# Performance work log

Hardware: AMD Instinct MI355X
Metric: run time of the kernel (lower is better)

## Reference

```python
import jax, jax.numpy as jnp
import numpy as np

E = 8        # numExperts
D = 1024     # d_model
F = 4096     # expert hidden = 4*d_model
T = 8192     # total tokens (sum of expertFrequency)


def setup_inputs() -> dict:
    key = jax.random.key(0)
    k0, k1, k2, k3, k4 = jax.random.split(key, 5)
    expertOrderedInput = jax.random.normal(k0, (T, D), dtype=jnp.float32)
    # Static equal split so the split sizes are jit-compatible.
    expertFrequency = jnp.full((E,), T // E, dtype=jnp.int64)
    s1 = 1.0 / np.sqrt(D)
    s2 = 1.0 / np.sqrt(F)
    w1 = jax.random.normal(k1, (E, D, F), dtype=jnp.float32) * s1
    b1 = jnp.zeros((E, F), dtype=jnp.float32)
    w2 = jax.random.normal(k2, (E, F, D), dtype=jnp.float32) * s2
    b2 = jnp.zeros((E, D), dtype=jnp.float32)
    return {"expertOrderedInput": expertOrderedInput,
            "expertFrequency": expertFrequency,
            "w1": w1, "b1": b1, "w2": w2, "b2": b2}


def reference(expertOrderedInput, expertFrequency, w1, b1, w2, b2):
    # expertOrderedInput: [T, D], tokens pre-sorted by expert.
    # expertFrequency is equal per expert (T/E each), so the
    # split-loop-cat in the torch module is exactly a grouped GEMM.
    e = w1.shape[0]
    t = expertOrderedInput.shape[0]
    x = expertOrderedInput.reshape(e, t // e, -1)            # [E, T/E, D]
    h = jax.nn.gelu(jnp.einsum('etd,edf->etf', x, w1) + b1[:, None, :])
    y = jnp.einsum('etf,efd->etd', h, w2) + b2[:, None, :]   # [E, T/E, D]
    return y.reshape(t, -1)                                   # cat along dim 0
```

## Files before the change

kernel.cpp:

```cpp
#include <hip/hip_runtime.h>

#define E_ 8
#define D_ 1024
#define F_ 4096
#define T_ 8192

typedef unsigned short u16;
typedef short bf16x8 __attribute__((ext_vector_type(8)));
typedef float f32x4 __attribute__((ext_vector_type(4)));
typedef unsigned short u16x8 __attribute__((ext_vector_type(8)));
typedef unsigned short u16x2 __attribute__((ext_vector_type(2)));

__device__ __forceinline__ u16 f2bf(float f) {
    unsigned u = __builtin_bit_cast(unsigned, f);
    u += 0x7fffu + ((u >> 16) & 1u);
    return (u16)(u >> 16);
}

__device__ __forceinline__ float gelu_fast(float x) {
    const float a = -2.885390082f * 0.7978845608028654f;
    const float b = a * 0.044715f;
    float u = x * x;
    float p = x * __builtin_fmaf(b, u, a);
    float e = exp2f(p);
    return x * __builtin_amdgcn_rcpf(1.0f + e);
}

__device__ __forceinline__ void async16(const void* g, void* l) {
    __builtin_amdgcn_global_load_lds(
        (const __attribute__((address_space(1))) unsigned int*)g,
        (__attribute__((address_space(3))) unsigned int*)l, 16, 0, 0);
}

__global__ void cvt_x(const float* __restrict__ in, u16* __restrict__ out) {
    int i = blockIdx.x * 256 + threadIdx.x;
    const float4* in4 = (const float4*)in;
    float4 a = in4[2 * i], b = in4[2 * i + 1];
    u16x8 o;
    o[0] = f2bf(a.x); o[1] = f2bf(a.y); o[2] = f2bf(a.z); o[3] = f2bf(a.w);
    o[4] = f2bf(b.x); o[5] = f2bf(b.y); o[6] = f2bf(b.z); o[7] = f2bf(b.w);
    *(u16x8*)(out + (size_t)i * 8) = o;
}

__global__ __launch_bounds__(256) void transpose_cvt(
    const float* __restrict__ src, u16* __restrict__ dst, int R, int C) {
    __shared__ float tile[32][129];
    int e = blockIdx.z;
    src += (size_t)e * R * C;
    dst += (size_t)e * R * C;
    int c0 = blockIdx.x * 32, r0 = blockIdx.y * 128;
    int tid = threadIdx.x;
    int lc = tid & 31, lr0 = tid >> 5;
#pragma unroll
    for (int i = 0; i < 16; ++i) {
        int r = lr0 + i * 8;
        tile[lc][r] = src[(size_t)(r0 + r) * C + c0 + lc];
    }
    __syncthreads();
    int sc = tid >> 6, sr = (tid & 63) * 2;
#pragma unroll
    for (int i = 0; i < 8; ++i) {
        int c = sc + i * 4;
        u16x2 v;
        v[0] = f2bf(tile[c][sr]);
        v[1] = f2bf(tile[c][sr + 1]);
        *(u16x2*)(dst + (size_t)(c0 + c) * R + r0 + sr) = v;
    }
}

template <int BN, int EPI, int NM, int NN>
__global__ __launch_bounds__(512, 2) void gemm2p(
    const u16* __restrict__ A,
    const u16* __restrict__ Bt,
    const float* __restrict__ bias,
    void* __restrict__ Cv,
    int Mpe, int N, int K) {
    constexpr int BM  = 256;
    constexpr int LA  = 2;
    constexpr int LB  = BN / 128;
    constexpr int MFR = 4;
    constexpr int NFR = BN / 32;
    constexpr int NH  = NFR / 2;
    constexpr int AELEM = 4 * BM * 32;
    constexpr int VMS = LA + LB;
    constexpr int RDS = MFR + 2 * NH;
    constexpr int LGP = MFR + NH;
    __shared__ u16 lds[AELEM + 4 * BN * 32];

    const int tid = threadIdx.x;
    const int w = tid >> 6, lane = tid & 63;
    const int lr = lane & 15, lg = lane >> 4;
    const int wm = w >> 1, wn = w & 1;

    constexpr int NWG = E_ * NM * NN;
    constexpr int PER = NWG / 8;
    const int bid = blockIdx.x;
    const int logical = (bid & 7) * PER + (bid >> 3);
    const int e   = logical / (NM * NN);
    const int rem = logical % (NM * NN);
    const int bn  = rem / NM;
    const int bm  = rem % NM;

    A    += (size_t)e * Mpe * K;
    Bt   += (size_t)e * N * K;
    bias += (size_t)e * N;
    const int n0 = bn * BN;
    const int m0 = bm * BM;
    const int NT = K >> 6;

    const char* gA[LA];
    const char* gB[LB];
    {
        int kch = (lane & 3) ^ ((lane >> 3) & 3);
#pragma unroll
        for (int i = 0; i < LA; ++i) {
            int row = i * 128 + w * 16 + (lane >> 2);
            gA[i] = (const char*)(A + (size_t)(m0 + row) * K + kch * 8);
        }
#pragma unroll
        for (int i = 0; i < LB; ++i) {
            int row = i * 128 + w * 16 + (lane >> 2);
            gB[i] = (const char*)(Bt + (size_t)(n0 + row) * K + kch * 8);
        }
    }
    char* ldsc = (char*)lds;

    auto stageA = [&](int t, int h) {
        size_t goff = (size_t)t * 128 + (size_t)h * 64;
        unsigned dst = (unsigned)((((t & 1) * 2 + h) * (BM * 64)) + w * 1024);
#pragma unroll
        for (int i = 0; i < LA; ++i)
            async16(gA[i] + goff, ldsc + dst + i * 8192);
    };
    auto stageB = [&](int t, int h) {
        size_t goff = (size_t)t * 128 + (size_t)h * 64;
        unsigned dst = (unsigned)(AELEM * 2 + (((t & 1) * 2 + h) * (BN * 64)) + w * 1024);
#pragma unroll
        for (int i = 0; i < LB; ++i)
            async16(gB[i] + goff, ldsc + dst + i * 8192);
    };

    f32x4 acc[MFR][NFR];
    const f32x4 zero = {0.f, 0.f, 0.f, 0.f};
#pragma unroll
    for (int i = 0; i < MFR; ++i)
#pragma unroll
        for (int j = 0; j < NFR; ++j) acc[i][j] = zero;

    const u16* SBb = lds + AELEM;
    const int arow = wm * 64 + lr;
    const int nbase = wn * (BN / 2) + lr;
    const int axor = (lg ^ ((arow >> 1) & 3)) * 8;
    const int bxor = (lg ^ ((nbase >> 1) & 3)) * 8;

    bf16x8 aC[MFR], aN[MFR], bloA[NH], bloB[NH], bhi[NH];

    stageA(0, 0); stageB(0, 0); stageA(0, 1); stageB(0, 1);
    if (NT > 1) { stageA(1, 0); stageB(1, 0); }
    if (NT > 1) asm volatile("s_waitcnt vmcnt(%0)" :: "i"(VMS) : "memory");
    else        asm volatile("s_waitcnt vmcnt(0)" ::: "memory");
    __builtin_amdgcn_s_barrier();
    __builtin_amdgcn_sched_barrier(0);
#pragma unroll
    for (int i = 0; i < MFR; ++i)
        aC[i] = *(const bf16x8*)(lds + (arow + i * 16) * 32 + axor);
#pragma unroll
    for (int j = 0; j < NH; ++j)
        bloA[j] = *(const bf16x8*)(SBb + (nbase + j * 16) * 32 + bxor);
    __builtin_amdgcn_sched_barrier(0);

#define MFMA_SUB(AARR, BARR, J0)                                              \
    __builtin_amdgcn_s_setprio(1);                                            \
    _Pragma("unroll")                                                         \
    for (int i = 0; i < MFR; ++i) {                                           \
        _Pragma("unroll")                                                     \
        for (int j = 0; j < NH; ++j)                                          \
            acc[i][(J0) + j] = __builtin_amdgcn_mfma_f32_16x16x32_bf16(       \
                AARR[i], BARR[j], acc[i][(J0) + j], 0, 0, 0);                 \
    }                                                                         \
    __builtin_amdgcn_s_setprio(0);

#pragma unroll 2
    for (int c = 0; c < NT; ++c) {
        const int bb = c & 1;
        const u16* SA1 = lds + (bb * 2 + 1) * (BM * 32);
        const u16* SB0 = SBb + (bb * 2 + 0) * (BN * 32);
        const u16* SB1 = SBb + (bb * 2 + 1) * (BN * 32);
        const u16* SA0n = lds + ((bb ^ 1) * 2) * (BM * 32);
        const u16* SB0n = SBb + ((bb ^ 1) * 2) * (BN * 32);
        const bool stg1 = (c + 1 < NT);
        const bool stg2 = (c + 2 < NT);

#pragma unroll
        for (int j = 0; j < NH; ++j)
            bhi[j] = *(const bf16x8*)(SB0 + (nbase + (NH + j) * 16) * 32 + bxor);
#pragma unroll
        for (int i = 0; i < MFR; ++i)
            aN[i] = *(const bf16x8*)(SA1 + (arow + i * 16) * 32 + axor);
#pragma unroll
        for (int j = 0; j < NH; ++j)
            bloB[j] = *(const bf16x8*)(SB1 + (nbase + j * 16) * 32 + bxor);
        if (stg1) { stageA(c + 1, 1); stageB(c + 1, 1); }
        __builtin_amdgcn_sched_barrier(0);
        asm volatile("s_waitcnt lgkmcnt(%0)" :: "i"(RDS) : "memory");
        __builtin_amdgcn_sched_barrier(0);
        MFMA_SUB(aC, bloA, 0);
        __builtin_amdgcn_sched_barrier(0);
        asm volatile("s_waitcnt lgkmcnt(%0)" :: "i"(LGP) : "memory");
        __builtin_amdgcn_sched_barrier(0);
        MFMA_SUB(aC, bhi, NH);
        __builtin_amdgcn_sched_barrier(0);
        if (stg1) asm volatile("s_waitcnt vmcnt(%0)" :: "i"(VMS) : "memory");
        else      asm volatile("s_waitcnt vmcnt(0)" ::: "memory");
        __builtin_amdgcn_s_barrier();
        __builtin_amdgcn_sched_barrier(0);

#pragma unroll
        for (int j = 0; j < NH; ++j)
            bhi[j] = *(const bf16x8*)(SB1 + (nbase + (NH + j) * 16) * 32 + bxor);
        if (stg1) {
#pragma unroll
            for (int i = 0; i < MFR; ++i)
                aC[i] = *(const bf16x8*)(SA0n + (arow + i * 16) * 32 + axor);
#pragma unroll
            for (int j = 0; j < NH; ++j)
                bloA[j] = *(const bf16x8*)(SB0n + (nbase + j * 16) * 32 + bxor);
        }
        if (stg2) { stageA(c + 2, 0); stageB(c + 2, 0); }
        __builtin_amdgcn_sched_barrier(0);
        if (stg1) asm volatile("s_waitcnt lgkmcnt(%0)" :: "i"(RDS) : "memory");
        else      asm volatile("s_waitcnt lgkmcnt(%0)" :: "i"(NH) : "memory");
        __builtin_amdgcn_sched_barrier(0);
        MFMA_SUB(aN, bloB, 0);
        __builtin_amdgcn_sched_barrier(0);
        if (stg1) asm volatile("s_waitcnt lgkmcnt(%0)" :: "i"(LGP) : "memory");
        else      asm volatile("s_waitcnt lgkmcnt(0)" ::: "memory");
        __builtin_amdgcn_sched_barrier(0);
        MFMA_SUB(aN, bhi, NH);
        __builtin_amdgcn_sched_barrier(0);
        if (stg2) asm volatile("s_waitcnt vmcnt(%0)" :: "i"(VMS) : "memory");
        else      asm volatile("s_waitcnt vmcnt(0)" ::: "memory");
        __builtin_amdgcn_s_barrier();
        __builtin_amdgcn_sched_barrier(0);
    }
#undef MFMA_SUB

    const int mb = m0 + wm * 64, nb = n0 + wn * (BN / 2);
    if constexpr (EPI == 1) {
        u16* C = (u16*)Cv + (size_t)e * Mpe * N;
#pragma unroll
        for (int i = 0; i < MFR; ++i) {
#pragma unroll
            for (int j = 0; j < NFR; ++j) {
                int col = nb + j * 16 + lr;
                float bv = bias[col];
                int row = mb + i * 16 + lg * 4;
#pragma unroll
                for (int t = 0; t < 4; ++t) {
                    float v = acc[i][j][t] + bv;
                    C[(size_t)(row + t) * N + col] = f2bf(gelu_fast(v));
                }
            }
        }
    } else {
        float* C = (float*)Cv + (size_t)e * Mpe * N;
#pragma unroll
        for (int i = 0; i < MFR; ++i) {
#pragma unroll
            for (int j = 0; j < NFR; ++j) {
                int col = nb + j * 16 + lr;
                float bv = bias[col];
                int row = mb + i * 16 + lg * 4;
#pragma unroll
                for (int t = 0; t < 4; ++t)
                    C[(size_t)(row + t) * N + col] = acc[i][j][t] + bv;
            }
        }
    }
}

extern "C" void kernel_launch(void* const* d_in, const int* in_sizes, int n_in,
                              void* d_out, int out_size, void* d_ws, size_t ws_size,
                              hipStream_t stream) {
    const float* X  = (const float*)d_in[0];
    const float* w1 = (const float*)d_in[2];
    const float* b1 = (const float*)d_in[3];
    const float* w2 = (const float*)d_in[4];
    const float* b2 = (const float*)d_in[5];
    float* out = (float*)d_out;

    const size_t XBF_B = (size_t)T_ * D_ * 2;
    const size_t WT_B  = (size_t)E_ * F_ * D_ * 2;
    const size_t H_B   = (size_t)T_ * F_ * 2;
    if (ws_size < XBF_B + WT_B + H_B) return;

    char* ws = (char*)d_ws;
    u16* Xbf = (u16*)ws;
    u16* Wt  = (u16*)(ws + XBF_B);
    u16* H   = (u16*)(ws + XBF_B + WT_B);

    cvt_x<<<dim3((T_ * D_) / 8 / 256), dim3(256), 0, stream>>>(X, Xbf);
    transpose_cvt<<<dim3(F_ / 32, D_ / 128, E_), dim3(256), 0, stream>>>(w1, Wt, D_, F_);
    gemm2p<256, 1, 4, 16><<<dim3(512), dim3(512), 0, stream>>>(
        Xbf, Wt, b1, H, T_ / E_, F_, D_);
    transpose_cvt<<<dim3(D_ / 32, F_ / 128, E_), dim3(256), 0, stream>>>(w2, Wt, F_, D_);
    gemm2p<128, 0, 4, 8><<<dim3(256), dim3(512), 0, stream>>>(
        H, Wt, b2, out, T_ / E_, D_, F_);
}
```

Baseline: 243.3 us.

## Fuse weight transpose and bf16 conversion into GEMM B-tile staging

Removes the two transpose_cvt kernels. The GEMMs now read fp32 weights directly from global memory into registers, convert them with v_cvt_pk_bf16_f32, and write them swizzled into LDS inside the software pipeline. This saves the extra passes over 256 MB of fp32 weights plus the write and re-read of the bf16 transposed copy. In exchange, each GEMM block re-reads fp32 weights (twice the bytes, once per M tile), loses the async global-to-LDS path for B, and adds register pressure and VALU work.

```diff
diff --git a/kernel.cpp b/kernel.cpp
--- a/kernel.cpp
+++ b/kernel.cpp
@@ -9,12 +9,18 @@
 typedef short bf16x8 __attribute__((ext_vector_type(8)));
 typedef float f32x4 __attribute__((ext_vector_type(4)));
 typedef unsigned short u16x8 __attribute__((ext_vector_type(8)));
-typedef unsigned short u16x2 __attribute__((ext_vector_type(2)));
+typedef unsigned int u32x4 __attribute__((ext_vector_type(4)));
 
 __device__ __forceinline__ u16 f2bf(float f) {
     unsigned u = __builtin_bit_cast(unsigned, f);
     u += 0x7fffu + ((u >> 16) & 1u);
     return (u16)(u >> 16);
+}
+
+__device__ __forceinline__ unsigned cvtpk(float a, float b) {
+    unsigned d;
+    asm("v_cvt_pk_bf16_f32 %0, %1, %2" : "=v"(d) : "v"(a), "v"(b));
+    return d;
 }
 
 __device__ __forceinline__ float gelu_fast(float x) {
@@ -42,49 +48,23 @@
     *(u16x8*)(out + (size_t)i * 8) = o;
 }
 
-__global__ __launch_bounds__(256) void transpose_cvt(
-    const float* __restrict__ src, u16* __restrict__ dst, int R, int C) {
-    __shared__ float tile[32][129];
-    int e = blockIdx.z;
-    src += (size_t)e * R * C;
-    dst += (size_t)e * R * C;
-    int c0 = blockIdx.x * 32, r0 = blockIdx.y * 128;
-    int tid = threadIdx.x;
-    int lc = tid & 31, lr0 = tid >> 5;
-#pragma unroll
-    for (int i = 0; i < 16; ++i) {
-        int r = lr0 + i * 8;
-        tile[lc][r] = src[(size_t)(r0 + r) * C + c0 + lc];
-    }
-    __syncthreads();
-    int sc = tid >> 6, sr = (tid & 63) * 2;
-#pragma unroll
-    for (int i = 0; i < 8; ++i) {
-        int c = sc + i * 4;
-        u16x2 v;
-        v[0] = f2bf(tile[c][sr]);
-        v[1] = f2bf(tile[c][sr + 1]);
-        *(u16x2*)(dst + (size_t)(c0 + c) * R + r0 + sr) = v;
-    }
-}
-
 template <int BN, int EPI, int NM, int NN>
-__global__ __launch_bounds__(512, 2) void gemm2p(
+__global__ __launch_bounds__(512, 2) void gemm2pw(
     const u16* __restrict__ A,
-    const u16* __restrict__ Bt,
+    const float* __restrict__ W,
     const float* __restrict__ bias,
     void* __restrict__ Cv,
     int Mpe, int N, int K) {
     constexpr int BM  = 256;
     constexpr int LA  = 2;
-    constexpr int LB  = BN / 128;
     constexpr int MFR = 4;
     constexpr int NFR = BN / 32;
     constexpr int NH  = NFR / 2;
+    constexpr int UNITS = BN / 128;
     constexpr int AELEM = 4 * BM * 32;
-    constexpr int VMS = LA + LB;
-    constexpr int RDS = MFR + 2 * NH;
-    constexpr int LGP = MFR + NH;
+    constexpr int RD  = MFR + 2 * NH;
+    constexpr int ENTRY = RD + UNITS;
+    constexpr int MID = MFR + NH;
     __shared__ u16 lds[AELEM + 4 * BN * 32];
 
     const int tid = threadIdx.x;
@@ -102,14 +82,13 @@
     const int bm  = rem % NM;
 
     A    += (size_t)e * Mpe * K;
-    Bt   += (size_t)e * N * K;
+    W    += (size_t)e * K * N;
     bias += (size_t)e * N;
     const int n0 = bn * BN;
     const int m0 = bm * BM;
     const int NT = K >> 6;
 
     const char* gA[LA];
-    const char* gB[LB];
     {
         int kch = (lane & 3) ^ ((lane >> 3) & 3);
 #pragma unroll
@@ -117,11 +96,6 @@
             int row = i * 128 + w * 16 + (lane >> 2);
             gA[i] = (const char*)(A + (size_t)(m0 + row) * K + kch * 8);
         }
-#pragma unroll
-        for (int i = 0; i < LB; ++i) {
-            int row = i * 128 + w * 16 + (lane >> 2);
-            gB[i] = (const char*)(Bt + (size_t)(n0 + row) * K + kch * 8);
-        }
     }
     char* ldsc = (char*)lds;
 
@@ -132,12 +106,34 @@
         for (int i = 0; i < LA; ++i)
             async16(gA[i] + goff, ldsc + dst + i * 8192);
     };
-    auto stageB = [&](int t, int h) {
-        size_t goff = (size_t)t * 128 + (size_t)h * 64;
-        unsigned dst = (unsigned)(AELEM * 2 + (((t & 1) * 2 + h) * (BN * 64)) + w * 1024);
-#pragma unroll
-        for (int i = 0; i < LB; ++i)
-            async16(gB[i] + goff, ldsc + dst + i * 8192);
+
+    const int NBLK = w & (BN / 64 - 1);
+    const int OCT0 = (w / (BN / 64)) * UNITS;
+    const int nl = NBLK * 64 + lane;
+    const float* Wb = W + n0 + nl;
+    float fb[UNITS * 8];
+
+    auto loadB = [&](int t, int h) {
+#pragma unroll
+        for (int u = 0; u < UNITS; ++u)
+#pragma unroll
+            for (int j = 0; j < 8; ++j) {
+                int row = t * 64 + h * 32 + (OCT0 + u) * 8 + j;
+                fb[u * 8 + j] = Wb[(size_t)row * N];
+            }
+    };
+    const int bwswz = ((nl >> 1) & 3);
+    auto writeB = [&](int t, int h) {
+        unsigned base = (unsigned)(AELEM * 2 + (((t & 1) * 2 + h) * (BN * 64)));
+#pragma unroll
+        for (int u = 0; u < UNITS; ++u) {
+            u32x4 v;
+            v[0] = cvtpk(fb[u * 8 + 0], fb[u * 8 + 1]);
+            v[1] = cvtpk(fb[u * 8 + 2], fb[u * 8 + 3]);
+            v[2] = cvtpk(fb[u * 8 + 4], fb[u * 8 + 5]);
+            v[3] = cvtpk(fb[u * 8 + 6], fb[u * 8 + 7]);
+            *(u32x4*)(ldsc + base + nl * 64 + (((OCT0 + u) ^ bwswz) << 4)) = v;
+        }
     };
 
     f32x4 acc[MFR][NFR];
@@ -155,10 +151,15 @@
 
     bf16x8 aC[MFR], aN[MFR], bloA[NH], bloB[NH], bhi[NH];
 
-    stageA(0, 0); stageB(0, 0); stageA(0, 1); stageB(0, 1);
-    if (NT > 1) { stageA(1, 0); stageB(1, 0); }
-    if (NT > 1) asm volatile("s_waitcnt vmcnt(%0)" :: "i"(VMS) : "memory");
-    else        asm volatile("s_waitcnt vmcnt(0)" ::: "memory");
+    loadB(0, 0);
+    asm volatile("s_waitcnt vmcnt(0)" ::: "memory");
+    writeB(0, 0);
+    loadB(0, 1);
+    asm volatile("s_waitcnt vmcnt(0)" ::: "memory");
+    writeB(0, 1);
+    loadB(1, 0);
+    stageA(0, 0); stageA(0, 1); stageA(1, 0);
+    asm volatile("s_waitcnt vmcnt(0)" ::: "memory");
     __builtin_amdgcn_s_barrier();
     __builtin_amdgcn_sched_barrier(0);
 #pragma unroll
@@ -180,7 +181,6 @@
     }                                                                         \
     __builtin_amdgcn_s_setprio(0);
 
-#pragma unroll 2
     for (int c = 0; c < NT; ++c) {
         const int bb = c & 1;
         const u16* SA1 = lds + (bb * 2 + 1) * (BM * 32);
@@ -191,6 +191,7 @@
         const bool stg1 = (c + 1 < NT);
         const bool stg2 = (c + 2 < NT);
 
+        if (stg1) { writeB(c + 1, 0); loadB(c + 1, 1); }
 #pragma unroll
         for (int j = 0; j < NH; ++j)
             bhi[j] = *(const bf16x8*)(SB0 + (nbase + (NH + j) * 16) * 32 + bxor);
@@ -200,21 +201,24 @@
 #pragma unroll
         for (int j = 0; j < NH; ++j)
             bloB[j] = *(const bf16x8*)(SB1 + (nbase + j * 16) * 32 + bxor);
-        if (stg1) { stageA(c + 1, 1); stageB(c + 1, 1); }
-        __builtin_amdgcn_sched_barrier(0);
-        asm volatile("s_waitcnt lgkmcnt(%0)" :: "i"(RDS) : "memory");
+        if (stg1) stageA(c + 1, 1);
+        __builtin_amdgcn_sched_barrier(0);
+        if (stg1) asm volatile("s_waitcnt lgkmcnt(%0)" :: "i"(ENTRY) : "memory");
+        else      asm volatile("s_waitcnt lgkmcnt(%0)" :: "i"(RD) : "memory");
         __builtin_amdgcn_sched_barrier(0);
         MFMA_SUB(aC, bloA, 0);
         __builtin_amdgcn_sched_barrier(0);
-        asm volatile("s_waitcnt lgkmcnt(%0)" :: "i"(LGP) : "memory");
+        asm volatile("s_waitcnt lgkmcnt(%0)" :: "i"(MID) : "memory");
         __builtin_amdgcn_sched_barrier(0);
         MFMA_SUB(aC, bhi, NH);
         __builtin_amdgcn_sched_barrier(0);
-        if (stg1) asm volatile("s_waitcnt vmcnt(%0)" :: "i"(VMS) : "memory");
+        if (stg1) asm volatile("s_waitcnt vmcnt(2)" ::: "memory");
         else      asm volatile("s_waitcnt vmcnt(0)" ::: "memory");
         __builtin_amdgcn_s_barrier();
         __builtin_amdgcn_sched_barrier(0);
 
+        if (stg1) writeB(c + 1, 1);
+        if (stg2) loadB(c + 2, 0);
 #pragma unroll
         for (int j = 0; j < NH; ++j)
             bhi[j] = *(const bf16x8*)(SB1 + (nbase + (NH + j) * 16) * 32 + bxor);
@@ -226,19 +230,19 @@
             for (int j = 0; j < NH; ++j)
                 bloA[j] = *(const bf16x8*)(SB0n + (nbase + j * 16) * 32 + bxor);
         }
-        if (stg2) { stageA(c + 2, 0); stageB(c + 2, 0); }
-        __builtin_amdgcn_sched_barrier(0);
-        if (stg1) asm volatile("s_waitcnt lgkmcnt(%0)" :: "i"(RDS) : "memory");
+        if (stg2) stageA(c + 2, 0);
+        __builtin_amdgcn_sched_barrier(0);
+        if (stg1) asm volatile("s_waitcnt lgkmcnt(%0)" :: "i"(ENTRY) : "memory");
         else      asm volatile("s_waitcnt lgkmcnt(%0)" :: "i"(NH) : "memory");
         __builtin_amdgcn_sched_barrier(0);
         MFMA_SUB(aN, bloB, 0);
         __builtin_amdgcn_sched_barrier(0);
-        if (stg1) asm volatile("s_waitcnt lgkmcnt(%0)" :: "i"(LGP) : "memory");
+        if (stg1) asm volatile("s_waitcnt lgkmcnt(%0)" :: "i"(MID) : "memory");
         else      asm volatile("s_waitcnt lgkmcnt(0)" ::: "memory");
         __builtin_amdgcn_sched_barrier(0);
         MFMA_SUB(aN, bhi, NH);
         __builtin_amdgcn_sched_barrier(0);
-        if (stg2) asm volatile("s_waitcnt vmcnt(%0)" :: "i"(VMS) : "memory");
+        if (stg2) asm volatile("s_waitcnt vmcnt(2)" ::: "memory");
         else      asm volatile("s_waitcnt vmcnt(0)" ::: "memory");
         __builtin_amdgcn_s_barrier();
         __builtin_amdgcn_sched_barrier(0);
@@ -290,20 +294,16 @@
     float* out = (float*)d_out;
 
     const size_t XBF_B = (size_t)T_ * D_ * 2;
-    const size_t WT_B  = (size_t)E_ * F_ * D_ * 2;
     const size_t H_B   = (size_t)T_ * F_ * 2;
-    if (ws_size < XBF_B + WT_B + H_B) return;
+    if (ws_size < XBF_B + H_B) return;
 
     char* ws = (char*)d_ws;
     u16* Xbf = (u16*)ws;
-    u16* Wt  = (u16*)(ws + XBF_B);
-    u16* H   = (u16*)(ws + XBF_B + WT_B);
+    u16* H   = (u16*)(ws + XBF_B);
 
     cvt_x<<<dim3((T_ * D_) / 8 / 256), dim3(256), 0, stream>>>(X, Xbf);
-    transpose_cvt<<<dim3(F_ / 32, D_ / 128, E_), dim3(256), 0, stream>>>(w1, Wt, D_, F_);
-    gemm2p<256, 1, 4, 16><<<dim3(512), dim3(512), 0, stream>>>(
-        Xbf, Wt, b1, H, T_ / E_, F_, D_);
-    transpose_cvt<<<dim3(D_ / 32, F_ / 128, E_), dim3(256), 0, stream>>>(w2, Wt, F_, D_);
-    gemm2p<128, 0, 4, 8><<<dim3(256), dim3(512), 0, stream>>>(
-        H, Wt, b2, out, T_ / E_, D_, F_);
-}
+    gemm2pw<256, 1, 4, 16><<<dim3(512), dim3(512), 0, stream>>>(
+        Xbf, w1, b1, H, T_ / E_, F_, D_);
+    gemm2pw<128, 0, 4, 8><<<dim3(256), dim3(512), 0, stream>>>(
+        H, w2, b2, out, T_ / E_, D_, F_);
+}
```

Result: slower. 635.0 us (+161.1%).
